# Performance work log

Hardware: AMD Instinct MI355X
Metric: run time of the kernel (lower is better)

Reference implementation:

```python
import jax, jax.numpy as jnp
import numpy as np

B, S, D, H = 8192, 45, 64, 8
HD = D // H          # head_dim = 8
FF = 4 * D           # FFN inner dim = 256


def _layernorm(x, g, b, eps=1e-5):
    m = x.mean(-1, keepdims=True)
    v = ((x - m) ** 2).mean(-1, keepdims=True)
    return (x - m) * jax.lax.rsqrt(v + eps) * g + b


def setup_inputs() -> dict:
    key = jax.random.key(0)
    ks = jax.random.split(key, 8)
    s = 1.0 / np.sqrt(D)
    sf = 1.0 / np.sqrt(FF)
    return {
        "x": jax.random.normal(ks[0], (B, S, D), jnp.float32),
        "Wq": jax.random.normal(ks[1], (D, D), jnp.float32) * s,
        "bq": jnp.zeros((D,), jnp.float32),
        "Wk": jax.random.normal(ks[2], (D, D), jnp.float32) * s,
        "bk": jnp.zeros((D,), jnp.float32),
        "Wv": jax.random.normal(ks[3], (D, D), jnp.float32) * s,
        "bv": jnp.zeros((D,), jnp.float32),
        "Wo": jax.random.normal(ks[4], (D, D), jnp.float32) * s,
        "bo": jnp.zeros((D,), jnp.float32),
        "ln1_g": jnp.ones((D,), jnp.float32),
        "ln1_b": jnp.zeros((D,), jnp.float32),
        "W1": jax.random.normal(ks[5], (D, FF), jnp.float32) * s,
        "b1": jnp.zeros((FF,), jnp.float32),
        "W2": jax.random.normal(ks[6], (FF, D), jnp.float32) * sf,
        "b2": jnp.zeros((D,), jnp.float32),
        "ln2_g": jnp.ones((D,), jnp.float32),
        "ln2_b": jnp.zeros((D,), jnp.float32),
    }


def reference(x, Wq, bq, Wk, bk, Wv, bv, Wo, bo, ln1_g, ln1_b, W1, b1, W2, b2, ln2_g, ln2_b):
    b, s, d = x.shape
    # sinusoidal positional encoding (PositionalEncoding(hidden_dim, max_len=45))
    pos = jnp.arange(s, dtype=jnp.float32)[:, None]
    div = jnp.exp(-jnp.log(jnp.float32(10000.0)) * jnp.arange(0, d, 2, dtype=jnp.float32) / d)
    ang = pos * div                              # [S, D/2]
    pe = jnp.zeros((s, d), x.dtype).at[:, 0::2].set(jnp.sin(ang)).at[:, 1::2].set(jnp.cos(ang))
    h = x + pe                                   # [B, S, D]
    residual = h
    # torch.nn.MultiheadAttention, batch_first=True, 8 heads, head_dim 8
    q = (h @ Wq + bq).reshape(b, s, H, HD).transpose(0, 2, 1, 3)  # [B,H,S,HD]
    k = (h @ Wk + bk).reshape(b, s, H, HD).transpose(0, 2, 1, 3)
    v = (h @ Wv + bv).reshape(b, s, H, HD).transpose(0, 2, 1, 3)
    scores = jnp.einsum('bhqd,bhkd->bhqk', q, k) / jnp.sqrt(jnp.float32(HD))
    attn = jax.nn.softmax(scores, axis=-1)
    o = jnp.einsum('bhqk,bhkd->bhqd', attn, v).transpose(0, 2, 1, 3).reshape(b, s, d)
    o = o @ Wo + bo
    # norm(out + alpha * residual), alpha = 1
    h2 = _layernorm(o + residual, ln1_g, ln1_b)
    # FFN: Linear -> ReLU -> Linear, residual + LayerNorm (standard transformer FFN)
    f = jax.nn.relu(h2 @ W1 + b1) @ W2 + b2
    return _layernorm(h2 + f, ln2_g, ln2_b)
```

## Files before the change

### kernel.cpp

```cpp
#include <hip/hip_runtime.h>
#include <math.h>

#define NB 8192
#define S_ 45
#define D_ 64
#define FF_ 256
#define LDH 68
#define HBS 72
#define KVS 68
#define FBH 136

typedef __attribute__((ext_vector_type(4))) float f32x4;
typedef __attribute__((ext_vector_type(8))) short s16x8;
typedef __attribute__((ext_vector_type(4))) short s16x4;
typedef __fp16 h16x2 __attribute__((ext_vector_type(2)));

#define WS_QKV 11520
#define WS_WO  36096
#define WS_W1  44288
#define WS_W2  77056

__device__ inline short f2bf(float f) {
    union { float f; unsigned u; } c; c.f = f;
    unsigned u = c.u;
    return (short)((u + 0x7FFFu + ((u >> 16) & 1u)) >> 16);
}
__device__ inline float bf2f(short s) {
    union { unsigned u; float f; } c;
    c.u = ((unsigned)(unsigned short)s) << 16;
    return c.f;
}

__global__ void prep_kernel(const float* __restrict__ Wq, const float* __restrict__ Wk,
                            const float* __restrict__ Wv, const float* __restrict__ Wo,
                            const float* __restrict__ W1, const float* __restrict__ W2,
                            void* __restrict__ ws) {
    float* pe   = (float*)ws;
    short* wqkv = (short*)((char*)ws + WS_QKV);
    short* wo   = (short*)((char*)ws + WS_WO);
    short* w1   = (short*)((char*)ws + WS_W1);
    short* w2   = (short*)((char*)ws + WS_W2);
    int i = blockIdx.x * 256 + threadIdx.x;
    if (i < S_ * D_) {
        int s = i / D_, d = i % D_;
        float div = expf(-logf(10000.0f) * (float)(d & ~1) / (float)D_);
        float ang = (float)s * div;
        pe[i] = (d & 1) ? cosf(ang) : sinf(ang);
    }
    if (i < 12288) {
        int n = i >> 6, k = i & 63;
        const float* W = (n < 64) ? Wq : (n < 128 ? Wk : Wv);
        wqkv[i] = f2bf(W[k * 64 + (n & 63)]);
    }
    if (i < 4096) {
        int n = i >> 6, k = i & 63;
        wo[i] = f2bf(Wo[k * 64 + n]);
    }
    if (i < 16384) {
        int n = i >> 6, k = i & 63;
        w1[i] = f2bf(W1[k * FF_ + n]);
        int n2 = i >> 8, k2 = i & 255;
        w2[i] = f2bf(W2[k2 * 64 + n2]);
    }
}

__launch_bounds__(512, 1)
__global__ void encoder_kernel(
    const float* __restrict__ x,
    const float* __restrict__ bq, const float* __restrict__ bk,
    const float* __restrict__ bv, const float* __restrict__ bo,
    const float* __restrict__ ln1g, const float* __restrict__ ln1b,
    const float* __restrict__ b1, const float* __restrict__ b2,
    const float* __restrict__ ln2g, const float* __restrict__ ln2b,
    const void* __restrict__ ws,
    float* __restrict__ out)
{
    const float* pe    = (const float*)ws;
    const short* wqkvT = (const short*)((const char*)ws + WS_QKV);
    const short* woT   = (const short*)((const char*)ws + WS_WO);
    const short* w1T   = (const short*)((const char*)ws + WS_W1);
    const short* w2T   = (const short*)((const char*)ws + WS_W2);

    __shared__ __align__(16) char pool[39168];
    short*   hb = (short*)pool;
    __fp16*  qh = (__fp16*)(pool + 6912);
    float*   kf = (float*)(pool + 13056);
    float*   vf = (float*)(pool + 26112);
    short*   ob = (short*)(pool + 6912);
    float*   t1 = (float*)(pool + 16384);
    short*   fb = (short*)(pool + 16384);
    float*   t2 = (float*)(pool + 16384);

    const int t = threadIdx.x;
    const int b = blockIdx.x;
    const int w = t >> 6, l = t & 63;
    const int lr = l & 15, lg = l >> 4;

    {
        const float4* x4 = (const float4*)(x + (size_t)b * (S_ * D_));
        const float4* p4 = (const float4*)pe;
        for (int i = t; i < S_ * D_ / 4; i += 512) {
            int r = i >> 4, c4 = (i & 15) << 2;
            float4 a = x4[i], p = p4[i];
            s16x4 hv16 = { f2bf(a.x + p.x), f2bf(a.y + p.y),
                           f2bf(a.z + p.z), f2bf(a.w + p.w) };
            *(s16x4*)&hb[r * HBS + c4] = hv16;
        }
        for (int i = t; i < 3 * HBS; i += 512) hb[45 * HBS + i] = 0;
    }
    __syncthreads();

    {
        const float SC2 = 0.35355339059327373f * 1.44269504088896340f;
        for (int id = w; id < 36; id += 8) {
            const int m0 = (id % 3) << 4, n0 = (id / 3) << 4;
            f32x4 acc = {0.f, 0.f, 0.f, 0.f};
            #pragma unroll
            for (int k0 = 0; k0 < 64; k0 += 32) {
                s16x8 af = *(const s16x8*)&hb[(m0 + lr) * HBS + k0 + lg * 8];
                s16x8 bf = *(const s16x8*)&wqkvT[(n0 + lr) * 64 + k0 + lg * 8];
                acc = __builtin_amdgcn_mfma_f32_16x16x32_bf16(af, bf, acc, 0, 0, 0);
            }
            if (n0 < 64) {
                const float bias = bq[n0 + lr];
                #pragma unroll
                for (int r = 0; r < 4; ++r)
                    qh[(m0 + lg * 4 + r) * 64 + n0 + lr] = (__fp16)((acc[r] + bias) * SC2);
            } else if (n0 < 128) {
                const int cc = n0 - 64 + lr;
                const float bias = bk[cc];
                #pragma unroll
                for (int r = 0; r < 4; ++r)
                    kf[(m0 + lg * 4 + r) * KVS + cc] = acc[r] + bias;
            } else {
                const int cc = n0 - 128 + lr;
                const float bias = bv[cc];
                #pragma unroll
                for (int r = 0; r < 4; ++r)
                    vf[(m0 + lg * 4 + r) * KVS + cc] = acc[r] + bias;
            }
        }
    }
    __syncthreads();

    {
        const bool act = (t < S_ * 8);
        s16x8 o16;
        int qr = 0, hd = 0;
        if (act) {
            qr = t >> 3; hd = (t & 7) << 3;
            float qv[8];
            {
                const h16x2* qp = (const h16x2*)&qh[qr * 64 + hd];
                #pragma unroll
                for (int j = 0; j < 4; ++j) {
                    h16x2 qq = qp[j];
                    qv[2 * j]     = (float)qq.x;
                    qv[2 * j + 1] = (float)qq.y;
                }
            }
            float o[8];
            #pragma unroll
            for (int j = 0; j < 8; ++j) o[j] = 0.f;
            float lsum = 0.f;
            #pragma unroll 3
            for (int k = 0; k < S_; ++k) {
                float4 k1 = *(const float4*)&kf[k * KVS + hd];
                float4 k2 = *(const float4*)&kf[k * KVS + hd + 4];
                float d = qv[0] * k1.x + qv[1] * k1.y + qv[2] * k1.z + qv[3] * k1.w +
                          qv[4] * k2.x + qv[5] * k2.y + qv[6] * k2.z + qv[7] * k2.w;
                float p = __builtin_amdgcn_exp2f(d);
                lsum += p;
                float4 v1 = *(const float4*)&vf[k * KVS + hd];
                float4 v2 = *(const float4*)&vf[k * KVS + hd + 4];
                o[0] += p * v1.x; o[1] += p * v1.y; o[2] += p * v1.z; o[3] += p * v1.w;
                o[4] += p * v2.x; o[5] += p * v2.y; o[6] += p * v2.z; o[7] += p * v2.w;
            }
            float inv = 1.0f / lsum;
            #pragma unroll
            for (int j = 0; j < 8; ++j) o16[j] = f2bf(o[j] * inv);
        }
        __syncthreads();
        if (act)
            *(s16x8*)&ob[qr * HBS + hd] = o16;
    }
    __syncthreads();

    {
        for (int id = w; id < 12; id += 8) {
            const int m0 = (id % 3) << 4, n0 = (id / 3) << 4;
            f32x4 acc = {0.f, 0.f, 0.f, 0.f};
            #pragma unroll
            for (int k0 = 0; k0 < 64; k0 += 32) {
                s16x8 af = *(const s16x8*)&ob[(m0 + lr) * HBS + k0 + lg * 8];
                s16x8 bf = *(const s16x8*)&woT[(n0 + lr) * 64 + k0 + lg * 8];
                acc = __builtin_amdgcn_mfma_f32_16x16x32_bf16(af, bf, acc, 0, 0, 0);
            }
            const int col = n0 + lr;
            const float bias = bo[col];
            #pragma unroll
            for (int r = 0; r < 4; ++r) {
                int row = m0 + lg * 4 + r;
                if (row < S_)
                    t1[row * LDH + col] = acc[r] + bias + bf2f(hb[row * HBS + col]);
            }
        }
    }
    __syncthreads();

    {
        const int wv = t >> 6, d = t & 63;
        const float g = ln1g[d], bb = ln1b[d];
        for (int i = 0; i < 6; ++i) {
            int r = wv + 8 * i;
            if (r < S_) {
                float v = t1[r * LDH + d];
                float s = v, s2 = v * v;
                #pragma unroll
                for (int off = 32; off; off >>= 1) {
                    s  += __shfl_xor(s, off);
                    s2 += __shfl_xor(s2, off);
                }
                float mean = s * (1.0f / 64.0f);
                float var  = s2 * (1.0f / 64.0f) - mean * mean;
                float nv = (v - mean) * rsqrtf(var + 1e-5f);
                hb[r * HBS + d] = f2bf(nv * g + bb);
            }
        }
    }
    __syncthreads();

    f32x4 facc0 = {0.f, 0.f, 0.f, 0.f};
    f32x4 facc1 = {0.f, 0.f, 0.f, 0.f};
    for (int hx = 0; hx < 2; ++hx) {
        for (int id = w; id < 24; id += 8) {
            const int m0 = (id % 3) << 4, nl = (id / 3) << 4;
            f32x4 acc = {0.f, 0.f, 0.f, 0.f};
            #pragma unroll
            for (int k0 = 0; k0 < 64; k0 += 32) {
                s16x8 af = *(const s16x8*)&hb[(m0 + lr) * HBS + k0 + lg * 8];
                s16x8 bf = *(const s16x8*)&w1T[(hx * 128 + nl + lr) * 64 + k0 + lg * 8];
                acc = __builtin_amdgcn_mfma_f32_16x16x32_bf16(af, bf, acc, 0, 0, 0);
            }
            const float bias = b1[hx * 128 + nl + lr];
            #pragma unroll
            for (int r = 0; r < 4; ++r) {
                int row = m0 + lg * 4 + r;
                if (row < S_)
                    fb[row * FBH + nl + lr] = f2bf(fmaxf(acc[r] + bias, 0.f));
            }
        }
        __syncthreads();
        {
            const int m0 = (w % 3) << 4, n0 = (w / 3) << 4;
            #pragma unroll
            for (int k0 = 0; k0 < 128; k0 += 32) {
                s16x8 af = *(const s16x8*)&fb[(m0 + lr) * FBH + k0 + lg * 8];
                s16x8 bf = *(const s16x8*)&w2T[(n0 + lr) * 256 + hx * 128 + k0 + lg * 8];
                facc0 = __builtin_amdgcn_mfma_f32_16x16x32_bf16(af, bf, facc0, 0, 0, 0);
            }
        }
        if (w < 4) {
            const int id = w + 8;
            const int m0 = (id % 3) << 4, n0 = (id / 3) << 4;
            #pragma unroll
            for (int k0 = 0; k0 < 128; k0 += 32) {
                s16x8 af = *(const s16x8*)&fb[(m0 + lr) * FBH + k0 + lg * 8];
                s16x8 bf = *(const s16x8*)&w2T[(n0 + lr) * 256 + hx * 128 + k0 + lg * 8];
                facc1 = __builtin_amdgcn_mfma_f32_16x16x32_bf16(af, bf, facc1, 0, 0, 0);
            }
        }
        __syncthreads();
    }
    {
        const int m0 = (w % 3) << 4, n0 = (w / 3) << 4;
        const int col = n0 + lr;
        const float bias = b2[col];
        #pragma unroll
        for (int r = 0; r < 4; ++r) {
            int row = m0 + lg * 4 + r;
            if (row < S_)
                t2[row * LDH + col] = facc0[r] + bias + bf2f(hb[row * HBS + col]);
        }
        if (w < 4) {
            const int id = w + 8;
            const int m1 = (id % 3) << 4, n1 = (id / 3) << 4;
            const int col1 = n1 + lr;
            const float bias1 = b2[col1];
            #pragma unroll
            for (int r = 0; r < 4; ++r) {
                int row = m1 + lg * 4 + r;
                if (row < S_)
                    t2[row * LDH + col1] = facc1[r] + bias1 + bf2f(hb[row * HBS + col1]);
            }
        }
    }
    __syncthreads();

    {
        const int wv = t >> 6, d = t & 63;
        const float g = ln2g[d], bb = ln2b[d];
        for (int i = 0; i < 6; ++i) {
            int r = wv + 8 * i;
            if (r < S_) {
                float v = t2[r * LDH + d];
                float s = v, s2 = v * v;
                #pragma unroll
                for (int off = 32; off; off >>= 1) {
                    s  += __shfl_xor(s, off);
                    s2 += __shfl_xor(s2, off);
                }
                float mean = s * (1.0f / 64.0f);
                float var  = s2 * (1.0f / 64.0f) - mean * mean;
                float nv = (v - mean) * rsqrtf(var + 1e-5f);
                out[(size_t)b * (S_ * D_) + r * 64 + d] = nv * g + bb;
            }
        }
    }
}

extern "C" void kernel_launch(void* const* d_in, const int* in_sizes, int n_in,
                              void* d_out, int out_size, void* d_ws, size_t ws_size,
                              hipStream_t stream) {
    const float* x    = (const float*)d_in[0];
    const float* Wq   = (const float*)d_in[1];
    const float* bq   = (const float*)d_in[2];
    const float* Wk   = (const float*)d_in[3];
    const float* bk   = (const float*)d_in[4];
    const float* Wv   = (const float*)d_in[5];
    const float* bv   = (const float*)d_in[6];
    const float* Wo   = (const float*)d_in[7];
    const float* bo   = (const float*)d_in[8];
    const float* ln1g = (const float*)d_in[9];
    const float* ln1b = (const float*)d_in[10];
    const float* W1   = (const float*)d_in[11];
    const float* b1   = (const float*)d_in[12];
    const float* W2   = (const float*)d_in[13];
    const float* b2   = (const float*)d_in[14];
    const float* ln2g = (const float*)d_in[15];
    const float* ln2b = (const float*)d_in[16];
    float* out = (float*)d_out;

    hipLaunchKernelGGL(prep_kernel, dim3(64), dim3(256), 0, stream,
                       Wq, Wk, Wv, Wo, W1, W2, d_ws);
    hipLaunchKernelGGL(encoder_kernel, dim3(NB), dim3(512), 0, stream,
                       x, bq, bk, bv, bo, ln1g, ln1b, b1, b2, ln2g, ln2b,
                       d_ws, out);
}
```

Baseline: 365.9 us.

## Compute per-head attention with bf16 MFMA instead of scalar FMA loops

```diff
diff --git a/kernel.cpp b/kernel.cpp
--- a/kernel.cpp
+++ b/kernel.cpp
@@ -7,13 +7,12 @@
 #define FF_ 256
 #define LDH 68
 #define HBS 72
-#define KVS 68
+#define VTS 56
 #define FBH 136
 
 typedef __attribute__((ext_vector_type(4))) float f32x4;
 typedef __attribute__((ext_vector_type(8))) short s16x8;
 typedef __attribute__((ext_vector_type(4))) short s16x4;
-typedef __fp16 h16x2 __attribute__((ext_vector_type(2)));
 
 #define WS_QKV 11520
 #define WS_WO  36096
@@ -81,20 +80,21 @@
     const short* w1T   = (const short*)((const char*)ws + WS_W1);
     const short* w2T   = (const short*)((const char*)ws + WS_W2);
 
-    __shared__ __align__(16) char pool[39168];
-    short*   hb = (short*)pool;
-    __fp16*  qh = (__fp16*)(pool + 6912);
-    float*   kf = (float*)(pool + 13056);
-    float*   vf = (float*)(pool + 26112);
-    short*   ob = (short*)(pool + 6912);
-    float*   t1 = (float*)(pool + 16384);
-    short*   fb = (short*)(pool + 16384);
-    float*   t2 = (float*)(pool + 16384);
+    __shared__ __align__(16) char pool[28800];
+    short* hb = (short*)pool;
+    short* qb = (short*)(pool + 6912);
+    short* kb = (short*)(pool + 13824);
+    short* vT = (short*)(pool + 20736);
+    short* ob = qb;
+    float* t1 = (float*)(pool + 13824);
+    short* fb = (short*)(pool + 13824);
+    float* t2 = (float*)(pool + 13824);
 
     const int t = threadIdx.x;
     const int b = blockIdx.x;
     const int w = t >> 6, l = t & 63;
     const int lr = l & 15, lg = l >> 4;
+    const s16x8 zero8 = {0, 0, 0, 0, 0, 0, 0, 0};
 
     {
         const float4* x4 = (const float4*)(x + (size_t)b * (S_ * D_));
@@ -125,64 +125,98 @@
                 const float bias = bq[n0 + lr];
                 #pragma unroll
                 for (int r = 0; r < 4; ++r)
-                    qh[(m0 + lg * 4 + r) * 64 + n0 + lr] = (__fp16)((acc[r] + bias) * SC2);
+                    qb[(m0 + lg * 4 + r) * HBS + n0 + lr] = f2bf((acc[r] + bias) * SC2);
             } else if (n0 < 128) {
                 const int cc = n0 - 64 + lr;
                 const float bias = bk[cc];
                 #pragma unroll
                 for (int r = 0; r < 4; ++r)
-                    kf[(m0 + lg * 4 + r) * KVS + cc] = acc[r] + bias;
+                    kb[(m0 + lg * 4 + r) * HBS + cc] = f2bf(acc[r] + bias);
             } else {
                 const int cc = n0 - 128 + lr;
                 const float bias = bv[cc];
-                #pragma unroll
-                for (int r = 0; r < 4; ++r)
-                    vf[(m0 + lg * 4 + r) * KVS + cc] = acc[r] + bias;
-            }
-        }
-    }
-    __syncthreads();
-
-    {
-        const bool act = (t < S_ * 8);
-        s16x8 o16;
-        int qr = 0, hd = 0;
-        if (act) {
-            qr = t >> 3; hd = (t & 7) << 3;
-            float qv[8];
-            {
-                const h16x2* qp = (const h16x2*)&qh[qr * 64 + hd];
-                #pragma unroll
-                for (int j = 0; j < 4; ++j) {
-                    h16x2 qq = qp[j];
-                    qv[2 * j]     = (float)qq.x;
-                    qv[2 * j + 1] = (float)qq.y;
+                s16x4 vv = { f2bf(acc[0] + bias), f2bf(acc[1] + bias),
+                             f2bf(acc[2] + bias), f2bf(acc[3] + bias) };
+                *(s16x4*)&vT[cc * VTS + m0 + lg * 4] = vv;
+            }
+        }
+    }
+    __syncthreads();
+
+    {
+        const int hd = w << 3;
+        s16x8 pv_b0 = *(const s16x8*)&vT[(hd + lr) * VTS + lg * 8];
+        s16x8 pv_b1 = (lg < 2) ? *(const s16x8*)&vT[(hd + lr) * VTS + 32 + lg * 8]
+                               : zero8;
+        f32x4 O[3];
+        #pragma unroll
+        for (int tn = 0; tn < 3; ++tn) {
+            s16x8 qbf = (lg == 0) ? *(const s16x8*)&qb[(tn * 16 + lr) * HBS + hd] : zero8;
+            f32x4 S[3];
+            #pragma unroll
+            for (int tm = 0; tm < 3; ++tm) {
+                s16x8 kaf = (lg == 0) ? *(const s16x8*)&kb[(tm * 16 + lr) * HBS + hd] : zero8;
+                f32x4 z = {0.f, 0.f, 0.f, 0.f};
+                S[tm] = __builtin_amdgcn_mfma_f32_16x16x32_bf16(kaf, qbf, z, 0, 0, 0);
+            }
+            float psum = 0.f;
+            #pragma unroll
+            for (int tm = 0; tm < 3; ++tm) {
+                #pragma unroll
+                for (int r = 0; r < 4; ++r) {
+                    float e = __builtin_amdgcn_exp2f(S[tm][r]);
+                    if (tm == 2) e = (lg * 4 + r >= 13) ? 0.f : e;
+                    S[tm][r] = e;
+                    psum += e;
                 }
             }
-            float o[8];
-            #pragma unroll
-            for (int j = 0; j < 8; ++j) o[j] = 0.f;
-            float lsum = 0.f;
-            #pragma unroll 3
-            for (int k = 0; k < S_; ++k) {
-                float4 k1 = *(const float4*)&kf[k * KVS + hd];
-                float4 k2 = *(const float4*)&kf[k * KVS + hd + 4];
-                float d = qv[0] * k1.x + qv[1] * k1.y + qv[2] * k1.z + qv[3] * k1.w +
-                          qv[4] * k2.x + qv[5] * k2.y + qv[6] * k2.z + qv[7] * k2.w;
-                float p = __builtin_amdgcn_exp2f(d);
-                lsum += p;
-                float4 v1 = *(const float4*)&vf[k * KVS + hd];
-                float4 v2 = *(const float4*)&vf[k * KVS + hd + 4];
-                o[0] += p * v1.x; o[1] += p * v1.y; o[2] += p * v1.z; o[3] += p * v1.w;
-                o[4] += p * v2.x; o[5] += p * v2.y; o[6] += p * v2.z; o[7] += p * v2.w;
-            }
-            float inv = 1.0f / lsum;
-            #pragma unroll
-            for (int j = 0; j < 8; ++j) o16[j] = f2bf(o[j] * inv);
+            float s = psum;
+            s += __shfl_xor(s, 16);
+            s += __shfl_xor(s, 32);
+            float inv = 1.0f / s;
+            unsigned pk0[3], pk1[3];
+            #pragma unroll
+            for (int tm = 0; tm < 3; ++tm) {
+                float a0 = S[tm][0] * inv, a1 = S[tm][1] * inv;
+                float a2 = S[tm][2] * inv, a3 = S[tm][3] * inv;
+                pk0[tm] = (__float_as_uint(a0) >> 16) | (__float_as_uint(a1) & 0xFFFF0000u);
+                pk1[tm] = (__float_as_uint(a2) >> 16) | (__float_as_uint(a3) & 0xFFFF0000u);
+            }
+            const int srcA = lr + ((lg & 1) << 5);
+            const int srcB = srcA + 16;
+            unsigned gA0[3], gA1[3], gB0[3], gB1[3];
+            #pragma unroll
+            for (int tm = 0; tm < 3; ++tm) {
+                gA0[tm] = (unsigned)__shfl((int)pk0[tm], srcA);
+                gA1[tm] = (unsigned)__shfl((int)pk1[tm], srcA);
+                gB0[tm] = (unsigned)__shfl((int)pk0[tm], srcB);
+                gB1[tm] = (unsigned)__shfl((int)pk1[tm], srcB);
+            }
+            const bool tm1 = (lg >> 1) != 0;
+            union { unsigned u[4]; s16x8 v; } a1c, a2c;
+            a1c.u[0] = tm1 ? gA0[1] : gA0[0];
+            a1c.u[1] = tm1 ? gA1[1] : gA1[0];
+            a1c.u[2] = tm1 ? gB0[1] : gB0[0];
+            a1c.u[3] = tm1 ? gB1[1] : gB1[0];
+            const bool lo = (lg < 2);
+            a2c.u[0] = lo ? gA0[2] : 0u;
+            a2c.u[1] = lo ? gA1[2] : 0u;
+            a2c.u[2] = lo ? gB0[2] : 0u;
+            a2c.u[3] = lo ? gB1[2] : 0u;
+            f32x4 z = {0.f, 0.f, 0.f, 0.f};
+            O[tn] = __builtin_amdgcn_mfma_f32_16x16x32_bf16(a1c.v, pv_b0, z, 0, 0, 0);
+            O[tn] = __builtin_amdgcn_mfma_f32_16x16x32_bf16(a2c.v, pv_b1, O[tn], 0, 0, 0);
         }
         __syncthreads();
-        if (act)
-            *(s16x8*)&ob[qr * HBS + hd] = o16;
+        if (lr < 8) {
+            #pragma unroll
+            for (int tn = 0; tn < 3; ++tn)
+                #pragma unroll
+                for (int r = 0; r < 4; ++r) {
+                    int row = tn * 16 + lg * 4 + r;
+                    if (row < S_) ob[row * HBS + hd + lr] = f2bf(O[tn][r]);
+                }
+        }
     }
     __syncthreads();
 
```

Measured after the change: 321.5 us. -12.1%, faster.
